# Kernel optimization log

Hardware: AMD Instinct MI355X
Metric: run time of the kernel (lower is better)

The kernel has to match this reference:

```python
import jax, jax.numpy as jnp
import numpy as np

N_NODES = 100000
N_EDGES = 1000000
D_IN = 64
D_HID = 64


def gcn_norm(edge_index, edge_weight, num_nodes):
    """PyG gcn_norm with add_self_loops=True, fill_value=1.0.
    Returns augmented (row, col, norm) including self loops."""
    loop = jnp.arange(num_nodes)
    row = jnp.concatenate([edge_index[0], loop])
    col = jnp.concatenate([edge_index[1], loop])
    ew = jnp.concatenate([edge_weight, jnp.ones((num_nodes,), edge_weight.dtype)])
    deg = jnp.zeros((num_nodes,), ew.dtype).at[col].add(ew)
    dinv = jnp.where(deg > 0, jax.lax.rsqrt(deg), 0.0).astype(ew.dtype)
    norm = dinv[row] * ew * dinv[col]  # [E + N]
    return row, col, norm


def gcn_conv(h, row, col, norm, W, b, num_nodes):
    """out[col] += norm * (h @ W)[row]; then add bias."""
    hw = h @ W  # [N, d_out] dense transform first (as PyG GCNConv)
    msg = norm[:, None] * hw[row]  # gather + scale  [E+N, d_out]
    out = jnp.zeros((num_nodes, W.shape[1]), h.dtype).at[col].add(msg)
    return out + b


def setup_inputs() -> dict:
    key = jax.random.key(0)
    ks = jax.random.split(key, 12)
    x = jax.random.normal(ks[0], (N_NODES, D_IN), jnp.float32)
    edge_index = jax.random.randint(ks[1], (2, N_EDGES), 0, N_NODES, jnp.int64)
    edge_weight = jax.random.uniform(ks[2], (N_EDGES,), jnp.float32)
    batch = jnp.zeros((N_NODES,), jnp.int64)

    def glorot(k, fan_in, fan_out):
        s = jnp.sqrt(6.0 / (fan_in + fan_out))
        return jax.random.uniform(k, (fan_in, fan_out), jnp.float32, -s, s)

    return {
        "x": x, "edge_index": edge_index, "edge_weight": edge_weight, "batch": batch,
        "W_in": glorot(ks[3], D_IN, D_HID), "b_in": jnp.zeros((D_HID,), jnp.float32),
        "W1": glorot(ks[4], D_HID, D_HID), "b1": jnp.zeros((D_HID,), jnp.float32),
        "W2": glorot(ks[5], D_HID, D_HID), "b2": jnp.zeros((D_HID,), jnp.float32),
        "Wf": glorot(ks[6], D_HID, 1), "bf": jnp.zeros((1,), jnp.float32),
    }


def reference(x, edge_index, edge_weight, batch, W_in, b_in, W1, b1, W2, b2, Wf, bf):
    n = x.shape[0]
    row, col, norm = gcn_norm(edge_index, edge_weight, n)  # shared across layers
    h = jax.nn.relu(gcn_conv(x, row, col, norm, W_in, b_in, n))
    h = jax.nn.relu(gcn_conv(h, row, col, norm, W1, b1, n) + h)
    h = jax.nn.relu(gcn_conv(h, row, col, norm, W2, b2, n) + h)
    out = gcn_conv(h, row, col, norm, Wf, bf, n)  # [N, 1]
    return out
```

## Files before the change

kernel.cpp:

```cpp
#include <hip/hip_runtime.h>

#define NN 100000
#define NE 1000000
#define D 64
#define BINB 8
#define BINSZ 256
#define NB ((NN + BINSZ - 1) / BINSZ)

using short8 = __attribute__((ext_vector_type(8))) short;
using f32x4  = __attribute__((ext_vector_type(4))) float;

__device__ __forceinline__ float bf2f(unsigned short u) {
    return __uint_as_float(((unsigned int)u) << 16);
}
__device__ __forceinline__ unsigned short f2bf(float f) {
    unsigned int u = __float_as_uint(f);
    u += 0x7fffu + ((u >> 16) & 1u);
    return (unsigned short)(u >> 16);
}

__global__ void bin_hist_kernel(const int* __restrict__ col, int* __restrict__ hist, int E) {
    __shared__ int h[NB];
    for (int i = threadIdx.x; i < NB; i += 256) h[i] = 0;
    __syncthreads();
    for (int e = blockIdx.x * 256 + threadIdx.x; e < E; e += gridDim.x * 256)
        atomicAdd(&h[col[e] >> BINB], 1);
    __syncthreads();
    for (int i = threadIdx.x; i < NB; i += 256)
        if (h[i]) atomicAdd(&hist[i], h[i]);
}

__global__ void bin_scan_kernel(const int* __restrict__ hist, int* __restrict__ binoff,
                                int* __restrict__ cursor) {
    __shared__ int s[512];
    int t = threadIdx.x;
    int v = (t < NB) ? hist[t] : 0;
    s[t] = v;
    __syncthreads();
#pragma unroll
    for (int o = 1; o < 512; o <<= 1) {
        int u = (t >= o) ? s[t - o] : 0;
        __syncthreads();
        s[t] += u;
        __syncthreads();
    }
    if (t < NB) {
        binoff[t] = s[t] - v;
        cursor[t] = s[t] - v;
    }
}

__global__ void bin_place_kernel(const int* __restrict__ row, const int* __restrict__ col,
                                 const float* __restrict__ ew, int* __restrict__ cursor,
                                 int2* __restrict__ ebin, int E) {
    __shared__ int h[NB];
    __shared__ int base[NB];
    for (int i = threadIdx.x; i < NB; i += 256) h[i] = 0;
    __syncthreads();
    int e0 = blockIdx.x * 256 + threadIdx.x;
    int stride = gridDim.x * 256;
    for (int e = e0; e < E; e += stride) atomicAdd(&h[col[e] >> BINB], 1);
    __syncthreads();
    for (int i = threadIdx.x; i < NB; i += 256) {
        int c = h[i];
        base[i] = c ? atomicAdd(&cursor[i], c) : 0;
    }
    __syncthreads();
    for (int i = threadIdx.x; i < NB; i += 256) h[i] = 0;
    __syncthreads();
    for (int e = e0; e < E; e += stride) {
        int c = col[e];
        int b = c >> BINB;
        int p = base[b] + atomicAdd(&h[b], 1);
        ebin[p] = make_int2(row[e] | ((c & (BINSZ - 1)) << 17), __float_as_int(ew[e]));
    }
}

__global__ __launch_bounds__(256) void bin_sort_kernel(const int* __restrict__ hist,
                                                       const int* __restrict__ binoff,
                                                       const int2* __restrict__ ebin,
                                                       int2* __restrict__ csr,
                                                       int* __restrict__ rowptr,
                                                       int* __restrict__ cnt,
                                                       float* __restrict__ dinv, int n) {
    __shared__ int   c256[BINSZ];
    __shared__ float s256[BINSZ];
    __shared__ int   scan[BINSZ];
    __shared__ int   woff[BINSZ];
    int b = blockIdx.x;
    int t = threadIdx.x;
    int sz = hist[b], off0 = binoff[b];
    c256[t] = 0;
    s256[t] = 0.f;
    __syncthreads();
    for (int i = t; i < sz; i += 256) {
        int2 ed = ebin[off0 + i];
        int cl = (ed.x >> 17) & 255;
        atomicAdd(&c256[cl], 1);
        atomicAdd(&s256[cl], __int_as_float(ed.y));
    }
    __syncthreads();
    int v = c256[t];
    scan[t] = v;
    __syncthreads();
#pragma unroll
    for (int o = 1; o < 256; o <<= 1) {
        int u = (t >= o) ? scan[t - o] : 0;
        __syncthreads();
        scan[t] += u;
        __syncthreads();
    }
    int excl = scan[t] - v;
    int c = b * BINSZ + t;
    if (c < n) {
        rowptr[c] = off0 + excl;
        cnt[c] = v;
        dinv[c] = rsqrtf(1.0f + s256[t]);
    }
    woff[t] = off0 + excl;
    __syncthreads();
    for (int i = t; i < sz; i += 256) {
        int2 ed = ebin[off0 + i];
        int cl = (ed.x >> 17) & 255;
        int p = atomicAdd(&woff[cl], 1);
        csr[p] = make_int2(ed.x & 0x1FFFF, ed.y);
    }
}

__global__ void wtrans3(const float* __restrict__ W0, const float* __restrict__ W1,
                        const float* __restrict__ W2, unsigned short* __restrict__ T0,
                        unsigned short* __restrict__ T1, unsigned short* __restrict__ T2) {
    int b = blockIdx.x >> 4;
    int i = (blockIdx.x & 15) * 256 + threadIdx.x;
    const float* W = (b == 0) ? W0 : (b == 1) ? W1 : W2;
    unsigned short* T = (b == 0) ? T0 : (b == 1) ? T1 : T2;
    int k = i >> 6, j = i & 63;
    T[j * 64 + k] = f2bf(W[k * 64 + j]);
}

template <int F32IN>
__global__ __launch_bounds__(256) void gemm_mfma(const void* __restrict__ Hv,
                                                 const unsigned short* __restrict__ Wt,
                                                 unsigned short* __restrict__ out16, int n) {
    int wave = threadIdx.x >> 6;
    int lane = threadIdx.x & 63;
    int r = lane & 15;
    int kg = lane >> 4;
    int base = blockIdx.x * 64 + wave * 16;
    int node = base + r;
    bool rv = node < n;

    short8 a[2];
    if (F32IN) {
        const float* hrow = (const float*)Hv + (size_t)(rv ? node : 0) * D;
#pragma unroll
        for (int kk = 0; kk < 2; ++kk) {
            float4 f0, f1;
            if (rv) {
                f0 = *(const float4*)(hrow + kk * 32 + kg * 8);
                f1 = *(const float4*)(hrow + kk * 32 + kg * 8 + 4);
            } else {
                f0 = make_float4(0.f, 0.f, 0.f, 0.f);
                f1 = f0;
            }
            short8 v;
            v[0] = (short)f2bf(f0.x); v[1] = (short)f2bf(f0.y);
            v[2] = (short)f2bf(f0.z); v[3] = (short)f2bf(f0.w);
            v[4] = (short)f2bf(f1.x); v[5] = (short)f2bf(f1.y);
            v[6] = (short)f2bf(f1.z); v[7] = (short)f2bf(f1.w);
            a[kk] = v;
        }
    } else {
        const unsigned short* hrow = (const unsigned short*)Hv + (size_t)(rv ? node : 0) * D;
#pragma unroll
        for (int kk = 0; kk < 2; ++kk) {
            short8 v;
            if (rv) v = *(const short8*)(hrow + kk * 32 + kg * 8);
            else    v = (short8){0, 0, 0, 0, 0, 0, 0, 0};
            a[kk] = v;
        }
    }

    f32x4 acc[4];
#pragma unroll
    for (int jt = 0; jt < 4; ++jt) acc[jt] = (f32x4){0.f, 0.f, 0.f, 0.f};

#pragma unroll
    for (int jt = 0; jt < 4; ++jt) {
        short8 b0 = *(const short8*)(Wt + ((jt * 16 + r) * 64 + kg * 8));
        short8 b1 = *(const short8*)(Wt + ((jt * 16 + r) * 64 + 32 + kg * 8));
        acc[jt] = __builtin_amdgcn_mfma_f32_16x16x32_bf16(a[0], b0, acc[jt], 0, 0, 0);
        acc[jt] = __builtin_amdgcn_mfma_f32_16x16x32_bf16(a[1], b1, acc[jt], 0, 0, 0);
    }

#pragma unroll
    for (int i = 0; i < 4; ++i) {
        int orow = base + 4 * kg + i;
        if (orow < n) {
            unsigned short* o = out16 + (size_t)orow * D + r;
#pragma unroll
            for (int jt = 0; jt < 4; ++jt) o[jt * 16] = f2bf(acc[jt][i]);
        }
    }
}

template <int HAS_RES>
__global__ void gather4_kernel(const int* __restrict__ rowptr, const int* __restrict__ cnt,
                               const int2* __restrict__ csr,
                               const ushort4* __restrict__ hw16,
                               const float* __restrict__ dinv, const float* __restrict__ b,
                               const unsigned short* __restrict__ hres,
                               unsigned short* __restrict__ hout, int n) {
    int c = blockIdx.x * 4 + (threadIdx.x >> 6);
    if (c >= n) return;
    int lane = threadIdx.x & 63;
    int q = lane >> 4;
    int fl = lane & 15;
    int start = rowptr[c];
    int deg = cnt[c];
    float dc = dinv[c];
    float ax = 0.f, ay = 0.f, az = 0.f, aw = 0.f;
    for (int base = 0; base < deg; base += 64) {
        int m = deg - base; if (m > 64) m = 64;
        int edr = 0; float wfull = 0.f;
        if (lane < m) {
            long long edb = __builtin_nontemporal_load(
                (const long long*)(csr + start + base + lane));
            edr = (int)(edb & 0xFFFFFFFFll);
            wfull = __int_as_float((int)(edb >> 32)) * dinv[edr] * dc;
        }
        int mr = (m + 15) & ~15;
        for (int t = 0; t < mr; t += 16) {
            int rr[4]; float wb[4]; ushort4 u[4];
#pragma unroll
            for (int p = 0; p < 4; ++p) {
                int tt = t + p * 4 + q;
                rr[p] = __shfl(edr, tt, 64);
                wb[p] = __shfl(wfull, tt, 64);
                u[p] = hw16[rr[p] * 16 + fl];
            }
#pragma unroll
            for (int p = 0; p < 4; ++p) {
                float w = wb[p];
                ax = fmaf(w, bf2f(u[p].x), ax);
                ay = fmaf(w, bf2f(u[p].y), ay);
                az = fmaf(w, bf2f(u[p].z), az);
                aw = fmaf(w, bf2f(u[p].w), aw);
            }
        }
    }
    ax += __shfl_xor(ax, 16, 64); ay += __shfl_xor(ay, 16, 64);
    az += __shfl_xor(az, 16, 64); aw += __shfl_xor(aw, 16, 64);
    ax += __shfl_xor(ax, 32, 64); ay += __shfl_xor(ay, 32, 64);
    az += __shfl_xor(az, 32, 64); aw += __shfl_xor(aw, 32, 64);
    if (lane < 16) {
        float dd = dc * dc;
        ushort4 su = hw16[c * 16 + fl];
        float4 bb = ((const float4*)b)[fl];
        float v0 = ax + dd * bf2f(su.x) + bb.x;
        float v1 = ay + dd * bf2f(su.y) + bb.y;
        float v2 = az + dd * bf2f(su.z) + bb.z;
        float v3 = aw + dd * bf2f(su.w) + bb.w;
        if (HAS_RES) {
            unsigned long long hrb = __builtin_nontemporal_load(
                (const unsigned long long*)(hres + (size_t)c * D + fl * 4));
            v0 += bf2f((unsigned short)(hrb & 0xFFFF));
            v1 += bf2f((unsigned short)((hrb >> 16) & 0xFFFF));
            v2 += bf2f((unsigned short)((hrb >> 32) & 0xFFFF));
            v3 += bf2f((unsigned short)((hrb >> 48) & 0xFFFF));
        }
        unsigned long long ob =
            (unsigned long long)f2bf(fmaxf(v0, 0.f)) |
            ((unsigned long long)f2bf(fmaxf(v1, 0.f)) << 16) |
            ((unsigned long long)f2bf(fmaxf(v2, 0.f)) << 32) |
            ((unsigned long long)f2bf(fmaxf(v3, 0.f)) << 48);
        __builtin_nontemporal_store(ob,
            (unsigned long long*)(hout + (size_t)c * D + fl * 4));
    }
}

__global__ void gather4_final_kernel(const int* __restrict__ rowptr, const int* __restrict__ cnt,
                                     const int2* __restrict__ csr,
                                     const ushort4* __restrict__ hw16,
                                     const float* __restrict__ dinv, const float* __restrict__ b,
                                     const unsigned short* __restrict__ hres,
                                     const float* __restrict__ Wf,
                                     float* __restrict__ hwf, int n) {
    int c = blockIdx.x * 4 + (threadIdx.x >> 6);
    if (c >= n) return;
    int lane = threadIdx.x & 63;
    int q = lane >> 4;
    int fl = lane & 15;
    int start = rowptr[c];
    int deg = cnt[c];
    float dc = dinv[c];
    float ax = 0.f, ay = 0.f, az = 0.f, aw = 0.f;
    for (int base = 0; base < deg; base += 64) {
        int m = deg - base; if (m > 64) m = 64;
        int edr = 0; float wfull = 0.f;
        if (lane < m) {
            long long edb = __builtin_nontemporal_load(
                (const long long*)(csr + start + base + lane));
            edr = (int)(edb & 0xFFFFFFFFll);
            wfull = __int_as_float((int)(edb >> 32)) * dinv[edr] * dc;
        }
        int mr = (m + 15) & ~15;
        for (int t = 0; t < mr; t += 16) {
            int rr[4]; float wb[4]; ushort4 u[4];
#pragma unroll
            for (int p = 0; p < 4; ++p) {
                int tt = t + p * 4 + q;
                rr[p] = __shfl(edr, tt, 64);
                wb[p] = __shfl(wfull, tt, 64);
                u[p] = hw16[rr[p] * 16 + fl];
            }
#pragma unroll
            for (int p = 0; p < 4; ++p) {
                float w = wb[p];
                ax = fmaf(w, bf2f(u[p].x), ax);
                ay = fmaf(w, bf2f(u[p].y), ay);
                az = fmaf(w, bf2f(u[p].z), az);
                aw = fmaf(w, bf2f(u[p].w), aw);
            }
        }
    }
    ax += __shfl_xor(ax, 16, 64); ay += __shfl_xor(ay, 16, 64);
    az += __shfl_xor(az, 16, 64); aw += __shfl_xor(aw, 16, 64);
    ax += __shfl_xor(ax, 32, 64); ay += __shfl_xor(ay, 32, 64);
    az += __shfl_xor(az, 32, 64); aw += __shfl_xor(aw, 32, 64);
    float dd = dc * dc;
    ushort4 su = hw16[c * 16 + fl];
    float4 bb = ((const float4*)b)[fl];
    unsigned long long hrb = __builtin_nontemporal_load(
        (const unsigned long long*)(hres + (size_t)c * D + fl * 4));
    float v0 = fmaxf(ax + dd * bf2f(su.x) + bb.x + bf2f((unsigned short)(hrb & 0xFFFF)), 0.f);
    float v1 = fmaxf(ay + dd * bf2f(su.y) + bb.y + bf2f((unsigned short)((hrb >> 16) & 0xFFFF)), 0.f);
    float v2 = fmaxf(az + dd * bf2f(su.z) + bb.z + bf2f((unsigned short)((hrb >> 32) & 0xFFFF)), 0.f);
    float v3 = fmaxf(aw + dd * bf2f(su.w) + bb.w + bf2f((unsigned short)((hrb >> 48) & 0xFFFF)), 0.f);
    float4 wf = ((const float4*)Wf)[fl];
    float part = v0 * wf.x + v1 * wf.y + v2 * wf.z + v3 * wf.w;
    part += __shfl_xor(part, 8, 16);
    part += __shfl_xor(part, 4, 16);
    part += __shfl_xor(part, 2, 16);
    part += __shfl_xor(part, 1, 16);
    if (lane == 0) hwf[c] = part;
}

__global__ void gather1_kernel(const int* __restrict__ rowptr, const int* __restrict__ cnt,
                               const int2* __restrict__ csr, const float* __restrict__ hwf,
                               const float* __restrict__ dinv, const float* __restrict__ bf,
                               float* __restrict__ out, int n) {
    int c = blockIdx.x * blockDim.x + threadIdx.x;
    if (c >= n) return;
    int s = rowptr[c];
    int d = cnt[c];
    float dc = dinv[c];
    float acc = 0.0f;
    for (int e = 0; e < d; ++e) {
        long long edb = __builtin_nontemporal_load((const long long*)(csr + s + e));
        int r = (int)(edb & 0xFFFFFFFFll);
        float w = __int_as_float((int)(edb >> 32)) * dinv[r] * dc;
        acc = fmaf(w, hwf[r], acc);
    }
    out[c] = acc + dc * dc * hwf[c] + bf[0];
}

extern "C" void kernel_launch(void* const* d_in, const int* in_sizes, int n_in,
                              void* d_out, int out_size, void* d_ws, size_t ws_size,
                              hipStream_t stream) {
    const float* x    = (const float*)d_in[0];
    const int*   ei   = (const int*)d_in[1];
    const float* ew   = (const float*)d_in[2];
    const float* W_in = (const float*)d_in[4];
    const float* b_in = (const float*)d_in[5];
    const float* W1   = (const float*)d_in[6];
    const float* b1   = (const float*)d_in[7];
    const float* W2   = (const float*)d_in[8];
    const float* b2   = (const float*)d_in[9];
    const float* Wf   = (const float*)d_in[10];
    const float* bf   = (const float*)d_in[11];
    float* out = (float*)d_out;

    const int E = NE, n = NN;
    const int* row = ei;
    const int* col = ei + E;

    char* ws = (char*)d_ws;
    size_t off = 0;
    auto alloc = [&](size_t nbytes) {
        void* p = (void*)(ws + off);
        off += ((nbytes + 255) / 256) * 256;
        return p;
    };
    int*   hist   = (int*)alloc((size_t)NB * 4);
    int*   binoff = (int*)alloc((size_t)NB * 4);
    int*   cursor = (int*)alloc((size_t)NB * 4);
    int2*  ebin   = (int2*)alloc((size_t)E * 8);
    int2*  csr    = (int2*)alloc((size_t)E * 8);
    int*   rowptr = (int*)alloc((size_t)n * 4);
    int*   cnt    = (int*)alloc((size_t)n * 4);
    float* dinv   = (float*)alloc((size_t)n * 4);
    unsigned short* hw16 = (unsigned short*)alloc((size_t)n * D * 2);
    unsigned short* hA   = (unsigned short*)alloc((size_t)n * D * 2);
    unsigned short* hB   = (unsigned short*)alloc((size_t)n * D * 2);
    float* hwf    = (float*)alloc((size_t)n * 4);
    unsigned short* Wt0 = (unsigned short*)alloc(D * D * 2);
    unsigned short* Wt1 = (unsigned short*)alloc(D * D * 2);
    unsigned short* Wt2 = (unsigned short*)alloc(D * D * 2);

    const int ngrid = (n + 255) / 256;
    const int mfma_grid = (n + 63) / 64;
    const int wave_grid = (n + 3) / 4;

    wtrans3<<<48, 256, 0, stream>>>(W_in, W1, W2, Wt0, Wt1, Wt2);

    hipMemsetAsync(hist, 0, NB * sizeof(int), stream);
    bin_hist_kernel<<<512, 256, 0, stream>>>(col, hist, E);
    bin_scan_kernel<<<1, 512, 0, stream>>>(hist, binoff, cursor);
    bin_place_kernel<<<512, 256, 0, stream>>>(row, col, ew, cursor, ebin, E);
    bin_sort_kernel<<<NB, 256, 0, stream>>>(hist, binoff, ebin, csr, rowptr, cnt, dinv, n);

    gemm_mfma<1><<<mfma_grid, 256, 0, stream>>>(x, Wt0, hw16, n);
    gather4_kernel<0><<<wave_grid, 256, 0, stream>>>(rowptr, cnt, csr, (const ushort4*)hw16,
                                                     dinv, b_in, nullptr, hA, n);

    gemm_mfma<0><<<mfma_grid, 256, 0, stream>>>(hA, Wt1, hw16, n);
    gather4_kernel<1><<<wave_grid, 256, 0, stream>>>(rowptr, cnt, csr, (const ushort4*)hw16,
                                                     dinv, b1, hA, hB, n);

    gemm_mfma<0><<<mfma_grid, 256, 0, stream>>>(hB, Wt2, hw16, n);
    gather4_final_kernel<<<wave_grid, 256, 0, stream>>>(rowptr, cnt, csr, (const ushort4*)hw16,
                                                        dinv, b2, hB, Wf, hwf, n);

    gather1_kernel<<<ngrid, 256, 0, stream>>>(rowptr, cnt, csr, hwf, dinv, bf, out, n);
}
```

Measured before the change: 349.6 us.

## Precompute normalized edge weights once, coalesce GEMM stores, fuse weight transpose

Adds a pass after CSR construction that folds dinv[row]*ew*dinv[col] into the stored edge weight, so the four gather kernels no longer do a random dinv[row] load per edge. The MFMA GEMM now stages its output tile in shared memory and writes 16-byte rows instead of scattered 2-byte stores. The weight transpose kernel is merged into the histogram kernel as extra blocks to save a launch. The cost is one extra read/write pass over the CSR array.

```diff
diff --git a/kernel.cpp b/kernel.cpp
--- a/kernel.cpp
+++ b/kernel.cpp
@@ -19,11 +19,24 @@
     return (unsigned short)(u >> 16);
 }
 
-__global__ void bin_hist_kernel(const int* __restrict__ col, int* __restrict__ hist, int E) {
+__global__ void bin_hist_wtrans(const int* __restrict__ col, int* __restrict__ hist, int E,
+                                const float* __restrict__ W0, const float* __restrict__ W1,
+                                const float* __restrict__ W2, unsigned short* __restrict__ T0,
+                                unsigned short* __restrict__ T1, unsigned short* __restrict__ T2) {
+    if (blockIdx.x >= 512) {
+        int b = blockIdx.x - 512;
+        int layer = b >> 4;
+        int i = (b & 15) * 256 + threadIdx.x;
+        const float* W = (layer == 0) ? W0 : (layer == 1) ? W1 : W2;
+        unsigned short* T = (layer == 0) ? T0 : (layer == 1) ? T1 : T2;
+        int k = i >> 6, j = i & 63;
+        T[j * 64 + k] = f2bf(W[k * 64 + j]);
+        return;
+    }
     __shared__ int h[NB];
     for (int i = threadIdx.x; i < NB; i += 256) h[i] = 0;
     __syncthreads();
-    for (int e = blockIdx.x * 256 + threadIdx.x; e < E; e += gridDim.x * 256)
+    for (int e = blockIdx.x * 256 + threadIdx.x; e < E; e += 512 * 256)
         atomicAdd(&h[col[e] >> BINB], 1);
     __syncthreads();
     for (int i = threadIdx.x; i < NB; i += 256)
@@ -123,31 +136,34 @@
         int2 ed = ebin[off0 + i];
         int cl = (ed.x >> 17) & 255;
         int p = atomicAdd(&woff[cl], 1);
-        csr[p] = make_int2(ed.x & 0x1FFFF, ed.y);
-    }
-}
-
-__global__ void wtrans3(const float* __restrict__ W0, const float* __restrict__ W1,
-                        const float* __restrict__ W2, unsigned short* __restrict__ T0,
-                        unsigned short* __restrict__ T1, unsigned short* __restrict__ T2) {
-    int b = blockIdx.x >> 4;
-    int i = (blockIdx.x & 15) * 256 + threadIdx.x;
-    const float* W = (b == 0) ? W0 : (b == 1) ? W1 : W2;
-    unsigned short* T = (b == 0) ? T0 : (b == 1) ? T1 : T2;
-    int k = i >> 6, j = i & 63;
-    T[j * 64 + k] = f2bf(W[k * 64 + j]);
+        csr[p] = ed;
+    }
+}
+
+__global__ void wscale_bin_kernel(const int* __restrict__ hist, const int* __restrict__ binoff,
+                                  int2* __restrict__ csr, const float* __restrict__ dinv) {
+    int b = blockIdx.x;
+    int sz = hist[b], off0 = binoff[b];
+    for (int i = threadIdx.x; i < sz; i += 256) {
+        int2 ed = csr[off0 + i];
+        int r = ed.x & 0x1FFFF;
+        int c = b * BINSZ + ((ed.x >> 17) & 255);
+        float w = __int_as_float(ed.y) * dinv[r] * dinv[c];
+        csr[off0 + i] = make_int2(r, __float_as_int(w));
+    }
 }
 
 template <int F32IN>
 __global__ __launch_bounds__(256) void gemm_mfma(const void* __restrict__ Hv,
                                                  const unsigned short* __restrict__ Wt,
                                                  unsigned short* __restrict__ out16, int n) {
+    __shared__ unsigned short st[4][16][72];
     int wave = threadIdx.x >> 6;
     int lane = threadIdx.x & 63;
     int r = lane & 15;
     int kg = lane >> 4;
-    int base = blockIdx.x * 64 + wave * 16;
-    int node = base + r;
+    int wbase = blockIdx.x * 64 + wave * 16;
+    int node = wbase + r;
     bool rv = node < n;
 
     short8 a[2];
@@ -194,12 +210,18 @@
     }
 
 #pragma unroll
-    for (int i = 0; i < 4; ++i) {
-        int orow = base + 4 * kg + i;
-        if (orow < n) {
-            unsigned short* o = out16 + (size_t)orow * D + r;
-#pragma unroll
-            for (int jt = 0; jt < 4; ++jt) o[jt * 16] = f2bf(acc[jt][i]);
+    for (int i = 0; i < 4; ++i)
+#pragma unroll
+        for (int jt = 0; jt < 4; ++jt)
+            st[wave][(kg << 2) | i][jt * 16 + r] = f2bf(acc[jt][i]);
+    int orow = lane >> 2;
+    int onode = wbase + orow;
+    if (onode < n) {
+#pragma unroll
+        for (int i = 0; i < 2; ++i) {
+            int seg = ((lane & 3) << 1) | i;
+            *(short8*)(out16 + (size_t)onode * D + seg * 8) =
+                *(const short8*)&st[wave][orow][seg * 8];
         }
     }
 }
@@ -218,30 +240,27 @@
     int fl = lane & 15;
     int start = rowptr[c];
     int deg = cnt[c];
-    float dc = dinv[c];
     float ax = 0.f, ay = 0.f, az = 0.f, aw = 0.f;
     for (int base = 0; base < deg; base += 64) {
         int m = deg - base; if (m > 64) m = 64;
-        int edr = 0; float wfull = 0.f;
-        if (lane < m) {
-            long long edb = __builtin_nontemporal_load(
-                (const long long*)(csr + start + base + lane));
-            edr = (int)(edb & 0xFFFFFFFFll);
-            wfull = __int_as_float((int)(edb >> 32)) * dinv[edr] * dc;
-        }
+        long long edb = 0;
+        if (lane < m)
+            edb = __builtin_nontemporal_load((const long long*)(csr + start + base + lane));
+        int edr = (int)(edb & 0xFFFFFFFFll);
+        int edw = (int)(edb >> 32);
         int mr = (m + 15) & ~15;
         for (int t = 0; t < mr; t += 16) {
-            int rr[4]; float wb[4]; ushort4 u[4];
+            int rr[4]; int wb[4]; ushort4 u[4];
 #pragma unroll
             for (int p = 0; p < 4; ++p) {
                 int tt = t + p * 4 + q;
                 rr[p] = __shfl(edr, tt, 64);
-                wb[p] = __shfl(wfull, tt, 64);
+                wb[p] = __shfl(edw, tt, 64);
                 u[p] = hw16[rr[p] * 16 + fl];
             }
 #pragma unroll
             for (int p = 0; p < 4; ++p) {
-                float w = wb[p];
+                float w = __int_as_float(wb[p]);
                 ax = fmaf(w, bf2f(u[p].x), ax);
                 ay = fmaf(w, bf2f(u[p].y), ay);
                 az = fmaf(w, bf2f(u[p].z), az);
@@ -254,7 +273,8 @@
     ax += __shfl_xor(ax, 32, 64); ay += __shfl_xor(ay, 32, 64);
     az += __shfl_xor(az, 32, 64); aw += __shfl_xor(aw, 32, 64);
     if (lane < 16) {
-        float dd = dc * dc;
+        float d = dinv[c];
+        float dd = d * d;
         ushort4 su = hw16[c * 16 + fl];
         float4 bb = ((const float4*)b)[fl];
         float v0 = ax + dd * bf2f(su.x) + bb.x;
@@ -293,30 +313,27 @@
     int fl = lane & 15;
     int start = rowptr[c];
     int deg = cnt[c];
-    float dc = dinv[c];
     float ax = 0.f, ay = 0.f, az = 0.f, aw = 0.f;
     for (int base = 0; base < deg; base += 64) {
         int m = deg - base; if (m > 64) m = 64;
-        int edr = 0; float wfull = 0.f;
-        if (lane < m) {
-            long long edb = __builtin_nontemporal_load(
-                (const long long*)(csr + start + base + lane));
-            edr = (int)(edb & 0xFFFFFFFFll);
-            wfull = __int_as_float((int)(edb >> 32)) * dinv[edr] * dc;
-        }
+        long long edb = 0;
+        if (lane < m)
+            edb = __builtin_nontemporal_load((const long long*)(csr + start + base + lane));
+        int edr = (int)(edb & 0xFFFFFFFFll);
+        int edw = (int)(edb >> 32);
         int mr = (m + 15) & ~15;
         for (int t = 0; t < mr; t += 16) {
-            int rr[4]; float wb[4]; ushort4 u[4];
+            int rr[4]; int wb[4]; ushort4 u[4];
 #pragma unroll
             for (int p = 0; p < 4; ++p) {
                 int tt = t + p * 4 + q;
                 rr[p] = __shfl(edr, tt, 64);
-                wb[p] = __shfl(wfull, tt, 64);
+                wb[p] = __shfl(edw, tt, 64);
                 u[p] = hw16[rr[p] * 16 + fl];
             }
 #pragma unroll
             for (int p = 0; p < 4; ++p) {
-                float w = wb[p];
+                float w = __int_as_float(wb[p]);
                 ax = fmaf(w, bf2f(u[p].x), ax);
                 ay = fmaf(w, bf2f(u[p].y), ay);
                 az = fmaf(w, bf2f(u[p].z), az);
@@ -328,7 +345,8 @@
     az += __shfl_xor(az, 16, 64); aw += __shfl_xor(aw, 16, 64);
     ax += __shfl_xor(ax, 32, 64); ay += __shfl_xor(ay, 32, 64);
     az += __shfl_xor(az, 32, 64); aw += __shfl_xor(aw, 32, 64);
-    float dd = dc * dc;
+    float d = dinv[c];
+    float dd = d * d;
     ushort4 su = hw16[c * 16 + fl];
     float4 bb = ((const float4*)b)[fl];
     unsigned long long hrb = __builtin_nontemporal_load(
@@ -354,14 +372,12 @@
     if (c >= n) return;
     int s = rowptr[c];
     int d = cnt[c];
-    float dc = dinv[c];
     float acc = 0.0f;
     for (int e = 0; e < d; ++e) {
         long long edb = __builtin_nontemporal_load((const long long*)(csr + s + e));
-        int r = (int)(edb & 0xFFFFFFFFll);
-        float w = __int_as_float((int)(edb >> 32)) * dinv[r] * dc;
-        acc = fmaf(w, hwf[r], acc);
-    }
+        acc = fmaf(__int_as_float((int)(edb >> 32)), hwf[(int)(edb & 0xFFFFFFFFll)], acc);
+    }
+    float dc = dinv[c];
     out[c] = acc + dc * dc * hwf[c] + bf[0];
 }
 
@@ -412,13 +428,12 @@
     const int mfma_grid = (n + 63) / 64;
     const int wave_grid = (n + 3) / 4;
 
-    wtrans3<<<48, 256, 0, stream>>>(W_in, W1, W2, Wt0, Wt1, Wt2);
-
     hipMemsetAsync(hist, 0, NB * sizeof(int), stream);
-    bin_hist_kernel<<<512, 256, 0, stream>>>(col, hist, E);
+    bin_hist_wtrans<<<560, 256, 0, stream>>>(col, hist, E, W_in, W1, W2, Wt0, Wt1, Wt2);
     bin_scan_kernel<<<1, 512, 0, stream>>>(hist, binoff, cursor);
     bin_place_kernel<<<512, 256, 0, stream>>>(row, col, ew, cursor, ebin, E);
     bin_sort_kernel<<<NB, 256, 0, stream>>>(hist, binoff, ebin, csr, rowptr, cnt, dinv, n);
+    wscale_bin_kernel<<<NB, 256, 0, stream>>>(hist, binoff, csr, dinv);
 
     gemm_mfma<1><<<mfma_grid, 256, 0, stream>>>(x, Wt0, hw16, n);
     gather4_kernel<0><<<wave_grid, 256, 0, stream>>>(rowptr, cnt, csr, (const ushort4*)hw16,
```

Result: no change. 344.9 us (-1.3%).
